# Optimization experiments

Hardware: AMD Instinct MI355X
Metric: run time of the kernel (lower is better)

Reference implementation:

```python
import jax, jax.numpy as jnp
import numpy as np

EMB = 1024
HEADS = 16
HEAD_DIM = EMB // HEADS
EPS = 1e-5


def setup_inputs() -> dict:
    key = jax.random.key(0)
    ks = jax.random.split(key, 10)
    B, T, D = 2, 2048, EMB
    s = 1.0 / np.sqrt(D)
    inp = {
        "x": jax.random.normal(ks[0], (B, T, D), dtype=jnp.float32),
        "wq": jax.random.normal(ks[1], (D, D), dtype=jnp.float32) * s,
        "bq": jnp.zeros((D,), jnp.float32),
        "wk": jax.random.normal(ks[2], (D, D), dtype=jnp.float32) * s,
        "bk": jnp.zeros((D,), jnp.float32),
        "wv": jax.random.normal(ks[3], (D, D), dtype=jnp.float32) * s,
        "bv": jnp.zeros((D,), jnp.float32),
        "wo": jax.random.normal(ks[4], (D, D), dtype=jnp.float32) * s,
        "bo": jnp.zeros((D,), jnp.float32),
        "gamma": jnp.ones((D,), jnp.float32),
        "beta": jnp.zeros((D,), jnp.float32),
    }
    return inp


def _attention(x, wq, bq, wk, bk, wv, bv, wo, bo, gamma, beta):
    B, T, D = x.shape
    H, Hd = HEADS, HEAD_DIM
    q = (x @ wq + bq).reshape(B, T, H, Hd)
    k = (x @ wk + bk).reshape(B, T, H, Hd)
    v = (x @ wv + bv).reshape(B, T, H, Hd)
    # scores: [B, H, T, T]
    scores = jnp.einsum("bthd,bshd->bhts", q, k) / np.sqrt(Hd)
    attn = jax.nn.softmax(scores, axis=-1)  # dropout is identity in eval
    ctx = jnp.einsum("bhts,bshd->bthd", attn, v).reshape(B, T, D)
    out = ctx @ wo + bo
    y = x + out  # residual (dropout identity)
    mu = jnp.mean(y, axis=-1, keepdims=True)
    var = jnp.var(y, axis=-1, keepdims=True)
    return (y - mu) * jax.lax.rsqrt(var + EPS) * gamma + beta


def reference(x, wq, bq, wk, bk, wv, bv, wo, bo, gamma, beta):
    return _attention(x, wq, bq, wk, bk, wv, bv, wo, bo, gamma, beta)
```

## Files before the change

### kernel.cpp

```cpp
#include <hip/hip_runtime.h>

#define BSZ   2
#define TSEQ  2048
#define DMOD  1024
#define NHEAD 16
#define HDIM  64
#define MROW  (BSZ*TSEQ)
#define LNEPS 1e-5f
#define QSCALE 0.18033688011f

typedef __bf16 bf16x8 __attribute__((ext_vector_type(8)));
typedef float  f32x4  __attribute__((ext_vector_type(4)));
typedef unsigned short us8 __attribute__((ext_vector_type(8)));
typedef unsigned short us4 __attribute__((ext_vector_type(4)));

__device__ __forceinline__ unsigned short f2bf(float f) {
    unsigned u = __float_as_uint(f);
    u += 0x7FFF + ((u >> 16) & 1);
    return (unsigned short)(u >> 16);
}
__device__ __forceinline__ float bf2f(unsigned short u) {
    return __uint_as_float((unsigned)u << 16);
}

__device__ __forceinline__ float fexp2(float x) {
#if __has_builtin(__builtin_amdgcn_exp2f)
    return __builtin_amdgcn_exp2f(x);
#else
    return __expf(x * 0.6931471805599453f);
#endif
}

__device__ __forceinline__ void gld_lds16(const void* g, void* l) {
    __builtin_amdgcn_global_load_lds(
        (const __attribute__((address_space(1))) unsigned int*)g,
        (__attribute__((address_space(3))) unsigned int*)l, 16, 0, 0);
}

__global__ __launch_bounds__(256) void prep_k(
    const float* __restrict__ x,
    const float* __restrict__ wq, const float* __restrict__ wk,
    const float* __restrict__ wv, const float* __restrict__ wo,
    unsigned short* __restrict__ Xb,
    unsigned short* __restrict__ WqkvT, unsigned short* __restrict__ WoT)
{
    const int tid = threadIdx.x;
    if (blockIdx.x < 2048) {
        const size_t i = ((size_t)blockIdx.x * 256 + tid) * 8;
        float4 a = *(const float4*)&x[i];
        float4 b = *(const float4*)&x[i + 4];
        union { unsigned short u[8]; uint4 v; } o;
        o.u[0]=f2bf(a.x); o.u[1]=f2bf(a.y); o.u[2]=f2bf(a.z); o.u[3]=f2bf(a.w);
        o.u[4]=f2bf(b.x); o.u[5]=f2bf(b.y); o.u[6]=f2bf(b.z); o.u[7]=f2bf(b.w);
        *(uint4*)&Xb[i] = o.v;
        return;
    }
    __shared__ float T[64][68];
    const int id = blockIdx.x - 2048;
    const int z  = id >> 8;
    const int bx = id & 15;
    const int by = (id >> 4) & 15;
    const float* W = (z == 0) ? wq : (z == 1) ? wk : (z == 2) ? wv : wo;
    unsigned short* Wt = (z < 3) ? (WqkvT + (size_t)z*1024*1024) : WoT;
    const int lr = tid >> 4, lc = (tid & 15) * 4;
    #pragma unroll
    for (int p = 0; p < 4; ++p) {
        const int kk = p*16 + lr;
        float4 v = *(const float4*)&W[(size_t)(by*64 + kk)*1024 + bx*64 + lc];
        T[lc+0][kk] = v.x; T[lc+1][kk] = v.y; T[lc+2][kk] = v.z; T[lc+3][kk] = v.w;
    }
    __syncthreads();
    #pragma unroll
    for (int p = 0; p < 2; ++p) {
        const int nl = p*32 + (tid >> 3);
        const int kb = (tid & 7) * 8;
        float4 a = *(const float4*)&T[nl][kb];
        float4 b = *(const float4*)&T[nl][kb+4];
        union { unsigned short u[8]; uint4 v; } o;
        o.u[0]=f2bf(a.x); o.u[1]=f2bf(a.y); o.u[2]=f2bf(a.z); o.u[3]=f2bf(a.w);
        o.u[4]=f2bf(b.x); o.u[5]=f2bf(b.y); o.u[6]=f2bf(b.z); o.u[7]=f2bf(b.w);
        *(uint4*)&Wt[(size_t)(bx*64 + nl)*1024 + by*64 + kb] = o.v;
    }
}

struct GemmFrags {
    const unsigned short* Ag[4]; const unsigned short* Bg[4];
    unsigned short *la[4], *lb[4];
    const unsigned short *ap[4][2], *bp[4][2];
};

__device__ __forceinline__ void gemm_setup(
    GemmFrags& F, unsigned short* As, unsigned short* Bs,
    const unsigned short* A, const unsigned short* Bt,
    int bm, int bn, int lda)
{
    const int tid  = threadIdx.x;
    const int wv   = tid >> 6;
    const int lane = tid & 63;
    const int quad = lane >> 4;
    const int l16  = lane & 15;
    const int wm   = wv & 1, wn = wv >> 1;
    const int r_l = lane >> 3;
    const int c_l = lane & 7;
    #pragma unroll
    for (int s = 0; s < 4; ++s) {
        const int i = wv*4 + s;
        const int R = i*8 + r_l;
        const int gc = (c_l ^ (R & 7)) * 8;
        F.Ag[s] = A  + (size_t)(bm + R)*lda + gc;
        F.Bg[s] = Bt + (size_t)(bn + R)*lda + gc;
        F.la[s] = As + i*512;
        F.lb[s] = Bs + i*512;
    }
    #pragma unroll
    for (int t = 0; t < 4; ++t)
        #pragma unroll
        for (int kh = 0; kh < 2; ++kh) {
            const int ra = wm*64 + t*16 + l16;
            const int rb = wn*64 + t*16 + l16;
            F.ap[t][kh] = &As[ra*64 + ((kh*4 + quad) ^ (ra & 7))*8];
            F.bp[t][kh] = &Bs[rb*64 + ((kh*4 + quad) ^ (rb & 7))*8];
        }
}

template<int SWAP>
__device__ __forceinline__ void gemm_kloop(
    GemmFrags& F, f32x4 (&acc)[4][4], int k_begin, int k_end)
{
    for (int k0 = k_begin; k0 < k_end; k0 += 64) {
        __syncthreads();
        #pragma unroll
        for (int s = 0; s < 4; ++s) {
            gld_lds16(F.Ag[s] + k0, F.la[s]);
            gld_lds16(F.Bg[s] + k0, F.lb[s]);
        }
        __syncthreads();
        #pragma unroll
        for (int kh = 0; kh < 2; ++kh) {
            bf16x8 af[4], bfr[4];
            #pragma unroll
            for (int t = 0; t < 4; ++t) {
                af[t]  = *(const bf16x8*)F.ap[t][kh];
                bfr[t] = *(const bf16x8*)F.bp[t][kh];
            }
            #pragma unroll
            for (int i = 0; i < 4; ++i)
                #pragma unroll
                for (int j = 0; j < 4; ++j)
                    acc[i][j] = SWAP
                        ? __builtin_amdgcn_mfma_f32_16x16x32_bf16(bfr[j], af[i], acc[i][j], 0, 0, 0)
                        : __builtin_amdgcn_mfma_f32_16x16x32_bf16(af[i], bfr[j], acc[i][j], 0, 0, 0);
        }
    }
}

__global__ __launch_bounds__(256) void gemm_qkv_k(
    const unsigned short* __restrict__ A, const unsigned short* __restrict__ Bt,
    const float* __restrict__ b0, const float* __restrict__ b1,
    const float* __restrict__ b2,
    unsigned short* __restrict__ oQ, unsigned short* __restrict__ oK,
    unsigned short* __restrict__ oV)
{
    __shared__ unsigned short As[128*64];
    __shared__ unsigned short Bs[128*64];
    const int tid  = threadIdx.x;
    const int wv   = tid >> 6;
    const int lane = tid & 63;
    const int quad = lane >> 4;
    const int l16  = lane & 15;
    const int wm   = wv & 1, wn = wv >> 1;
    const int bm = blockIdx.y * 128, bn = blockIdx.x * 128;

    GemmFrags F;
    gemm_setup(F, As, Bs, A, Bt, bm, bn, 1024);

    f32x4 acc[4][4];
    #pragma unroll
    for (int i = 0; i < 4; ++i)
        #pragma unroll
        for (int j = 0; j < 4; ++j) acc[i][j] = (f32x4){0.f,0.f,0.f,0.f};

    const int seg = bn >> 10;
    const float* bias = (seg == 0) ? b0 : (seg == 1) ? b1 : b2;
    const int cb = bn & 1023;

    if (seg < 2) {
        gemm_kloop<1>(F, acc, 0, 1024);
        unsigned short* O = (seg == 0) ? oQ : oK;
        const float sc = (seg == 0) ? QSCALE : 1.0f;
        #pragma unroll
        for (int mt = 0; mt < 4; ++mt) {
            const int m = bm + wm*64 + mt*16 + l16;
            #pragma unroll
            for (int nt = 0; nt < 4; ++nt) {
                const int n0 = cb + wn*64 + nt*16 + quad*4;
                const f32x4 bs = *(const f32x4*)&bias[n0];
                us4 o;
                #pragma unroll
                for (int r = 0; r < 4; ++r) o[r] = f2bf((acc[mt][nt][r] + bs[r]) * sc);
                *(us4*)&O[(size_t)m*1024 + n0] = o;
            }
        }
    } else {
        gemm_kloop<0>(F, acc, 0, 1024);
        #pragma unroll
        for (int nt = 0; nt < 4; ++nt) {
            const int ch = cb + wn*64 + nt*16 + l16;
            const float bs = bias[ch];
            #pragma unroll
            for (int mt = 0; mt < 4; ++mt) {
                const int grow0 = bm + wm*64 + mt*16 + quad*4;
                us4 o;
                #pragma unroll
                for (int r = 0; r < 4; ++r) o[r] = f2bf(acc[mt][nt][r] + bs);
                *(us4*)&oV[(size_t)ch*MROW + grow0] = o;
            }
        }
    }
}

__global__ __launch_bounds__(256) void gemm_proj_k(
    const unsigned short* __restrict__ A, const unsigned short* __restrict__ Bt,
    unsigned short* __restrict__ P)
{
    __shared__ unsigned short As[128*64];
    __shared__ unsigned short Bs[128*64];
    const int tid  = threadIdx.x;
    const int wv   = tid >> 6;
    const int lane = tid & 63;
    const int quad = lane >> 4;
    const int l16  = lane & 15;
    const int wm   = wv & 1, wn = wv >> 1;
    const int bm = blockIdx.y * 128, bn = blockIdx.x * 128;
    const int kz = blockIdx.z;

    GemmFrags F;
    gemm_setup(F, As, Bs, A, Bt, bm, bn, 1024);

    f32x4 acc[4][4];
    #pragma unroll
    for (int i = 0; i < 4; ++i)
        #pragma unroll
        for (int j = 0; j < 4; ++j) acc[i][j] = (f32x4){0.f,0.f,0.f,0.f};

    gemm_kloop<1>(F, acc, kz*512, kz*512 + 512);

    unsigned short* O = P + (size_t)kz*MROW*1024;
    #pragma unroll
    for (int mt = 0; mt < 4; ++mt) {
        const int m = bm + wm*64 + mt*16 + l16;
        #pragma unroll
        for (int nt = 0; nt < 4; ++nt) {
            const int n0 = bn + wn*64 + nt*16 + quad*4;
            us4 o;
            #pragma unroll
            for (int r = 0; r < 4; ++r) o[r] = f2bf(acc[mt][nt][r]);
            *(us4*)&O[(size_t)m*1024 + n0] = o;
        }
    }
}

__global__ __launch_bounds__(256, 2) void attn_k(
    const unsigned short* __restrict__ Qg,
    const unsigned short* __restrict__ Kg,
    const unsigned short* __restrict__ Vtg,
    unsigned short* __restrict__ CTX)
{
    __shared__ __align__(16) char lds_raw[51200];
    unsigned short* Qs = (unsigned short*)lds_raw;
    unsigned short* Ks = (unsigned short*)(lds_raw + 18432);
    unsigned short* Vs = (unsigned short*)(lds_raw + 34816);
    float* Od = (float*)lds_raw;
    float* Ld = (float*)(lds_raw + 34816);

    const int tid  = threadIdx.x;
    const int wv   = tid >> 6;
    const int lane = tid & 63;
    const int quad = lane >> 4;
    const int l16  = lane & 15;
    const int wq   = wv & 1;
    const int wk   = wv >> 1;
    const int qb   = blockIdx.x * 128;
    const int h    = blockIdx.y;
    const int b    = blockIdx.z;

    {
        const int row = tid & 127, cb = (tid >> 7) * 32;
        const unsigned short* Qrow = Qg + ((size_t)(b*TSEQ + qb + row))*DMOD + h*HDIM + cb;
        #pragma unroll
        for (int j = 0; j < 4; ++j)
            *(us8*)&Qs[row*72 + cb + j*8] = *(const us8*)&Qrow[j*8];
    }
    __syncthreads();
    bf16x8 qf[4][2];
    #pragma unroll
    for (int nt = 0; nt < 4; ++nt)
        #pragma unroll
        for (int kh = 0; kh < 2; ++kh)
            qf[nt][kh] = *(const bf16x8*)&Qs[(wq*64 + nt*16 + l16)*72 + kh*32 + quad*8];

    const int sr = lane >> 3;
    const int sc = lane & 7;
    const bool isK = (wv < 2);
    const int half = wv & 1;
    const unsigned short* gbase;
    unsigned int goff[8];
    unsigned short* ldst;
    if (isK) {
        gbase = Kg + ((size_t)(b*TSEQ + half*1024))*DMOD + h*HDIM;
        #pragma unroll
        for (int s = 0; s < 8; ++s) {
            const int R = s*8 + sr;
            const int gc = sc ^ ((R ^ (R >> 2)) & 7);
            goff[s] = (unsigned)(R*DMOD + gc*8);
        }
        ldst = Ks + half*4096;
    } else {
        gbase = Vtg + ((size_t)(h*HDIM))*MROW + b*TSEQ + half*1024;
        #pragma unroll
        for (int s = 0; s < 8; ++s) {
            const int D = s*8 + sr;
            const int gc = sc ^ (D & 7);
            goff[s] = (unsigned)(D*MROW + gc*8);
        }
        ldst = Vs + half*4096;
    }
    const size_t gstep = isK ? (size_t)64*DMOD : (size_t)64;

    const int rowA_l = (l16 >> 2)*8 + (l16 & 3);
    const int rowB_l = rowA_l + 4;
    const int swA = (rowA_l ^ (rowA_l >> 2)) & 7;
    const int swB = (rowB_l ^ (rowB_l >> 2)) & 7;
    const unsigned short* KsW = Ks + wk*4096;
    const unsigned short* VsW = Vs + wk*4096;

    bf16x8 onef;
    { union { unsigned short u[8]; bf16x8 v; } o1;
      #pragma unroll
      for (int i = 0; i < 8; ++i) o1.u[i] = 0x3F80;
      onef = o1.v; }

    f32x4 oacc[4][4];
    f32x4 lacc[4];
    #pragma unroll
    for (int dt = 0; dt < 4; ++dt)
        #pragma unroll
        for (int nt = 0; nt < 4; ++nt) oacc[dt][nt] = (f32x4){0.f,0.f,0.f,0.f};
    #pragma unroll
    for (int nt = 0; nt < 4; ++nt) lacc[nt] = (f32x4){0.f,0.f,0.f,0.f};

    for (int it = 0; it < 16; ++it) {
        __syncthreads();
        #pragma unroll
        for (int s = 0; s < 8; ++s)
            gld_lds16(gbase + (size_t)it*gstep + goff[s], ldst + s*512);
        __syncthreads();

        #pragma unroll
        for (int gl = 0; gl < 2; ++gl) {
            const int rA = gl*32 + rowA_l;
            const int rB = gl*32 + rowB_l;
            bf16x8 ka0 = *(const bf16x8*)&KsW[rA*64 + ((quad     ^ swA))*8];
            bf16x8 ka1 = *(const bf16x8*)&KsW[rA*64 + (((4+quad) ^ swA))*8];
            bf16x8 kb0 = *(const bf16x8*)&KsW[rB*64 + ((quad     ^ swB))*8];
            bf16x8 kb1 = *(const bf16x8*)&KsW[rB*64 + (((4+quad) ^ swB))*8];
            bf16x8 vf[4];
            #pragma unroll
            for (int dt = 0; dt < 4; ++dt)
                vf[dt] = *(const bf16x8*)&VsW[(dt*16 + l16)*64 + ((gl*4 + quad) ^ (l16 & 7))*8];

            #pragma unroll
            for (int nt = 0; nt < 4; ++nt) {
                f32x4 z = (f32x4){0.f,0.f,0.f,0.f};
                z = __builtin_amdgcn_mfma_f32_16x16x32_bf16(ka0, qf[nt][0], z, 0, 0, 0);
                f32x4 sA = __builtin_amdgcn_mfma_f32_16x16x32_bf16(ka1, qf[nt][1], z, 0, 0, 0);
                z = (f32x4){0.f,0.f,0.f,0.f};
                z = __builtin_amdgcn_mfma_f32_16x16x32_bf16(kb0, qf[nt][0], z, 0, 0, 0);
                f32x4 sB = __builtin_amdgcn_mfma_f32_16x16x32_bf16(kb1, qf[nt][1], z, 0, 0, 0);

                float eA[4], eB[4];
                #pragma unroll
                for (int r = 0; r < 4; ++r) { eA[r] = fexp2(sA[r]); eB[r] = fexp2(sB[r]); }
                union { unsigned d[4]; bf16x8 v; } up;
                up.d[0] = __builtin_amdgcn_perm(__float_as_uint(eA[1]), __float_as_uint(eA[0]), 0x07060302);
                up.d[1] = __builtin_amdgcn_perm(__float_as_uint(eA[3]), __float_as_uint(eA[2]), 0x07060302);
                up.d[2] = __builtin_amdgcn_perm(__float_as_uint(eB[1]), __float_as_uint(eB[0]), 0x07060302);
                up.d[3] = __builtin_amdgcn_perm(__float_as_uint(eB[3]), __float_as_uint(eB[2]), 0x07060302);
                const bf16x8 pf = up.v;

                lacc[nt] = __builtin_amdgcn_mfma_f32_16x16x32_bf16(onef, pf, lacc[nt], 0, 0, 0);
                #pragma unroll
                for (int dt = 0; dt < 4; ++dt)
                    oacc[dt][nt] = __builtin_amdgcn_mfma_f32_16x16x32_bf16(vf[dt], pf, oacc[dt][nt], 0, 0, 0);
            }
        }
    }

    __syncthreads();
    if (wk == 0) {
        float* od = Od + wq*64*68;
        #pragma unroll
        for (int nt = 0; nt < 4; ++nt) {
            #pragma unroll
            for (int dt = 0; dt < 4; ++dt)
                *(f32x4*)&od[(nt*16 + l16)*68 + dt*16 + quad*4] = oacc[dt][nt];
            if (quad == 0) Ld[wq*64 + nt*16 + l16] = lacc[nt][0];
        }
    }
    __syncthreads();
    if (wk == 1) {
        const float* od = Od + wq*64*68;
        #pragma unroll
        for (int nt = 0; nt < 4; ++nt) {
            const float l = Ld[wq*64 + nt*16 + l16] + lacc[nt][0];
            const float inv = 1.f / l;
            const int q = qb + wq*64 + nt*16 + l16;
            unsigned short* crow = CTX + ((size_t)(b*TSEQ + q))*DMOD + h*HDIM;
            #pragma unroll
            for (int dt = 0; dt < 4; ++dt) {
                f32x4 p = *(const f32x4*)&od[(nt*16 + l16)*68 + dt*16 + quad*4];
                us4 o;
                #pragma unroll
                for (int r = 0; r < 4; ++r) o[r] = f2bf((p[r] + oacc[dt][nt][r]) * inv);
                *(us4*)&crow[dt*16 + quad*4] = o;
            }
        }
    }
}

__global__ __launch_bounds__(256) void red_ln_k(
    const float* __restrict__ x, const unsigned short* __restrict__ P,
    const float* __restrict__ bo,
    const float* __restrict__ gamma, const float* __restrict__ beta,
    float* __restrict__ out)
{
    __shared__ float rs[4], rss[4];
    const int row = blockIdx.x;
    const int tid = threadIdx.x;
    const int c = tid * 4;
    const float4 xv = *(const float4*)&x[(size_t)row*DMOD + c];
    const us4 p0 = *(const us4*)&P[(size_t)row*DMOD + c];
    const us4 p1 = *(const us4*)&P[(size_t)(MROW + row)*DMOD + c];
    const float4 bv4 = *(const float4*)&bo[c];
    const float v0 = xv.x + bf2f(p0[0]) + bf2f(p1[0]) + bv4.x;
    const float v1 = xv.y + bf2f(p0[1]) + bf2f(p1[1]) + bv4.y;
    const float v2 = xv.z + bf2f(p0[2]) + bf2f(p1[2]) + bv4.z;
    const float v3 = xv.w + bf2f(p0[3]) + bf2f(p1[3]) + bv4.w;
    float s  = v0 + v1 + v2 + v3;
    float ss = v0*v0 + v1*v1 + v2*v2 + v3*v3;
    #pragma unroll
    for (int o = 32; o > 0; o >>= 1) {
        s  += __shfl_down(s,  o, 64);
        ss += __shfl_down(ss, o, 64);
    }
    if ((tid & 63) == 0) { rs[tid >> 6] = s; rss[tid >> 6] = ss; }
    __syncthreads();
    s  = rs[0] + rs[1] + rs[2] + rs[3];
    ss = rss[0] + rss[1] + rss[2] + rss[3];
    const float mean = s * (1.f/DMOD);
    const float var  = ss * (1.f/DMOD) - mean*mean;
    const float rstd = rsqrtf(var + LNEPS);
    const float4 gv = *(const float4*)&gamma[c];
    const float4 bv = *(const float4*)&beta[c];
    float4 o;
    o.x = (v0 - mean)*rstd*gv.x + bv.x;
    o.y = (v1 - mean)*rstd*gv.y + bv.y;
    o.z = (v2 - mean)*rstd*gv.z + bv.z;
    o.w = (v3 - mean)*rstd*gv.w + bv.w;
    *(float4*)&out[(size_t)row*DMOD + c] = o;
}

extern "C" void kernel_launch(void* const* d_in, const int* in_sizes, int n_in,
                              void* d_out, int out_size, void* d_ws, size_t ws_size,
                              hipStream_t stream) {
    const float* x     = (const float*)d_in[0];
    const float* wq    = (const float*)d_in[1];
    const float* bq    = (const float*)d_in[2];
    const float* wk    = (const float*)d_in[3];
    const float* bk    = (const float*)d_in[4];
    const float* wvp   = (const float*)d_in[5];
    const float* bvp   = (const float*)d_in[6];
    const float* wo    = (const float*)d_in[7];
    const float* bo    = (const float*)d_in[8];
    const float* gamma = (const float*)d_in[9];
    const float* beta  = (const float*)d_in[10];
    float* out = (float*)d_out;

    unsigned short* Xb    = (unsigned short*)d_ws;
    unsigned short* WqkvT = Xb    + (size_t)MROW*DMOD;
    unsigned short* WoT   = WqkvT + (size_t)3072*1024;
    unsigned short* Qb    = WoT   + (size_t)1024*1024;
    unsigned short* Kb    = Qb    + (size_t)MROW*DMOD;
    unsigned short* VtG   = Kb    + (size_t)MROW*DMOD;
    unsigned short* CTXb  = VtG   + (size_t)DMOD*MROW;
    unsigned short* Pp    = Qb;

    prep_k<<<3072, 256, 0, stream>>>(x, wq, wk, wvp, wo, Xb, WqkvT, WoT);

    gemm_qkv_k<<<dim3(3072/128, MROW/128), 256, 0, stream>>>(
        Xb, WqkvT, bq, bk, bvp, Qb, Kb, VtG);

    attn_k<<<dim3(TSEQ/128, NHEAD, BSZ), 256, 0, stream>>>(Qb, Kb, VtG, CTXb);

    gemm_proj_k<<<dim3(DMOD/128, MROW/128, 2), 256, 0, stream>>>(CTXb, WoT, Pp);

    red_ln_k<<<MROW, 256, 0, stream>>>(x, Pp, bo, gamma, beta, out);
}
```

Before: 201.0 us.

## Double-buffer GEMM k-loop with 32-wide LDS stages to overlap loads and MFMA

Splits each 64-wide K step of the QKV and projection GEMMs into two 32-wide stages held in two LDS buffers. The global-to-LDS load of the next stage is issued before the MFMA work on the current stage, so memory latency can overlap with compute instead of being serialized behind a barrier. The LDS swizzle and fragment offsets are reworked for the 32-column stage layout, and total LDS use stays the same. The loop still has two barriers per 64 of K, and the narrower stages mean fewer MFMAs between syncs.

New measurement: 206.1 us. +2.6%, slower.

```diff
diff --git a/kernel.cpp b/kernel.cpp
--- a/kernel.cpp
+++ b/kernel.cpp
@@ -84,14 +84,13 @@
 }
 
 struct GemmFrags {
-    const unsigned short* Ag[4]; const unsigned short* Bg[4];
-    unsigned short *la[4], *lb[4];
-    const unsigned short *ap[4][2], *bp[4][2];
+    const unsigned short* Ag[2]; const unsigned short* Bg[2];
+    int ldso[2];
+    int apo[4], bpo[4];
 };
 
 __device__ __forceinline__ void gemm_setup(
-    GemmFrags& F, unsigned short* As, unsigned short* Bs,
-    const unsigned short* A, const unsigned short* Bt,
+    GemmFrags& F, const unsigned short* A, const unsigned short* Bt,
     int bm, int bn, int lda)
 {
     const int tid  = threadIdx.x;
@@ -100,57 +99,69 @@
     const int quad = lane >> 4;
     const int l16  = lane & 15;
     const int wm   = wv & 1, wn = wv >> 1;
-    const int r_l = lane >> 3;
-    const int c_l = lane & 7;
-    #pragma unroll
-    for (int s = 0; s < 4; ++s) {
-        const int i = wv*4 + s;
-        const int R = i*8 + r_l;
-        const int gc = (c_l ^ (R & 7)) * 8;
+    const int r_l = lane >> 2;
+    const int c_l = lane & 3;
+    #pragma unroll
+    for (int s = 0; s < 2; ++s) {
+        const int R = wv*32 + s*16 + r_l;
+        const int gc = (c_l ^ (r_l & 3)) * 8;
         F.Ag[s] = A  + (size_t)(bm + R)*lda + gc;
         F.Bg[s] = Bt + (size_t)(bn + R)*lda + gc;
-        F.la[s] = As + i*512;
-        F.lb[s] = Bs + i*512;
-    }
-    #pragma unroll
-    for (int t = 0; t < 4; ++t)
-        #pragma unroll
-        for (int kh = 0; kh < 2; ++kh) {
-            const int ra = wm*64 + t*16 + l16;
-            const int rb = wn*64 + t*16 + l16;
-            F.ap[t][kh] = &As[ra*64 + ((kh*4 + quad) ^ (ra & 7))*8];
-            F.bp[t][kh] = &Bs[rb*64 + ((kh*4 + quad) ^ (rb & 7))*8];
-        }
+        F.ldso[s] = (wv*32 + s*16)*32;
+    }
+    #pragma unroll
+    for (int t = 0; t < 4; ++t) {
+        const int ra = wm*64 + t*16 + l16;
+        const int rb = wn*64 + t*16 + l16;
+        F.apo[t] = ra*32 + ((quad ^ (ra & 3))*8);
+        F.bpo[t] = rb*32 + ((quad ^ (rb & 3))*8);
+    }
+}
+
+__device__ __forceinline__ void gemm_load(
+    GemmFrags& F, unsigned short* SA, unsigned short* SB, int k0)
+{
+    #pragma unroll
+    for (int s = 0; s < 2; ++s) {
+        gld_lds16(F.Ag[s] + k0, SA + F.ldso[s]);
+        gld_lds16(F.Bg[s] + k0, SB + F.ldso[s]);
+    }
+}
+
+template<int SWAP>
+__device__ __forceinline__ void gemm_compute(
+    GemmFrags& F, const unsigned short* SA, const unsigned short* SB,
+    f32x4 (&acc)[4][4])
+{
+    bf16x8 af[4], bfr[4];
+    #pragma unroll
+    for (int t = 0; t < 4; ++t) {
+        af[t]  = *(const bf16x8*)(SA + F.apo[t]);
+        bfr[t] = *(const bf16x8*)(SB + F.bpo[t]);
+    }
+    #pragma unroll
+    for (int i = 0; i < 4; ++i)
+        #pragma unroll
+        for (int j = 0; j < 4; ++j)
+            acc[i][j] = SWAP
+                ? __builtin_amdgcn_mfma_f32_16x16x32_bf16(bfr[j], af[i], acc[i][j], 0, 0, 0)
+                : __builtin_amdgcn_mfma_f32_16x16x32_bf16(af[i], bfr[j], acc[i][j], 0, 0, 0);
 }
 
 template<int SWAP>
 __device__ __forceinline__ void gemm_kloop(
-    GemmFrags& F, f32x4 (&acc)[4][4], int k_begin, int k_end)
-{
-    for (int k0 = k_begin; k0 < k_end; k0 += 64) {
+    GemmFrags& F, unsigned short* S, f32x4 (&acc)[4][4], int kb, int ke)
+{
+    unsigned short* A0 = S;         unsigned short* A1 = S + 4096;
+    unsigned short* B0 = S + 8192;  unsigned short* B1 = S + 12288;
+    gemm_load(F, A0, B0, kb);
+    for (int k0 = kb; k0 < ke; k0 += 64) {
         __syncthreads();
-        #pragma unroll
-        for (int s = 0; s < 4; ++s) {
-            gld_lds16(F.Ag[s] + k0, F.la[s]);
-            gld_lds16(F.Bg[s] + k0, F.lb[s]);
-        }
+        gemm_load(F, A1, B1, k0 + 32);
+        gemm_compute<SWAP>(F, A0, B0, acc);
         __syncthreads();
-        #pragma unroll
-        for (int kh = 0; kh < 2; ++kh) {
-            bf16x8 af[4], bfr[4];
-            #pragma unroll
-            for (int t = 0; t < 4; ++t) {
-                af[t]  = *(const bf16x8*)F.ap[t][kh];
-                bfr[t] = *(const bf16x8*)F.bp[t][kh];
-            }
-            #pragma unroll
-            for (int i = 0; i < 4; ++i)
-                #pragma unroll
-                for (int j = 0; j < 4; ++j)
-                    acc[i][j] = SWAP
-                        ? __builtin_amdgcn_mfma_f32_16x16x32_bf16(bfr[j], af[i], acc[i][j], 0, 0, 0)
-                        : __builtin_amdgcn_mfma_f32_16x16x32_bf16(af[i], bfr[j], acc[i][j], 0, 0, 0);
-        }
+        if (k0 + 64 < ke) gemm_load(F, A0, B0, k0 + 64);
+        gemm_compute<SWAP>(F, A1, B1, acc);
     }
 }
 
@@ -161,8 +172,7 @@
     unsigned short* __restrict__ oQ, unsigned short* __restrict__ oK,
     unsigned short* __restrict__ oV)
 {
-    __shared__ unsigned short As[128*64];
-    __shared__ unsigned short Bs[128*64];
+    __shared__ unsigned short S[4*4096];
     const int tid  = threadIdx.x;
     const int wv   = tid >> 6;
     const int lane = tid & 63;
@@ -172,7 +182,7 @@
     const int bm = blockIdx.y * 128, bn = blockIdx.x * 128;
 
     GemmFrags F;
-    gemm_setup(F, As, Bs, A, Bt, bm, bn, 1024);
+    gemm_setup(F, A, Bt, bm, bn, 1024);
 
     f32x4 acc[4][4];
     #pragma unroll
@@ -185,7 +195,7 @@
     const int cb = bn & 1023;
 
     if (seg < 2) {
-        gemm_kloop<1>(F, acc, 0, 1024);
+        gemm_kloop<1>(F, S, acc, 0, 1024);
         unsigned short* O = (seg == 0) ? oQ : oK;
         const float sc = (seg == 0) ? QSCALE : 1.0f;
         #pragma unroll
@@ -202,7 +212,7 @@
             }
         }
     } else {
-        gemm_kloop<0>(F, acc, 0, 1024);
+        gemm_kloop<0>(F, S, acc, 0, 1024);
         #pragma unroll
         for (int nt = 0; nt < 4; ++nt) {
             const int ch = cb + wn*64 + nt*16 + l16;
@@ -223,8 +233,7 @@
     const unsigned short* __restrict__ A, const unsigned short* __restrict__ Bt,
     unsigned short* __restrict__ P)
 {
-    __shared__ unsigned short As[128*64];
-    __shared__ unsigned short Bs[128*64];
+    __shared__ unsigned short S[4*4096];
     const int tid  = threadIdx.x;
     const int wv   = tid >> 6;
     const int lane = tid & 63;
@@ -235,7 +244,7 @@
     const int kz = blockIdx.z;
 
     GemmFrags F;
-    gemm_setup(F, As, Bs, A, Bt, bm, bn, 1024);
+    gemm_setup(F, A, Bt, bm, bn, 1024);
 
     f32x4 acc[4][4];
     #pragma unroll
@@ -243,7 +252,7 @@
         #pragma unroll
         for (int j = 0; j < 4; ++j) acc[i][j] = (f32x4){0.f,0.f,0.f,0.f};
 
-    gemm_kloop<1>(F, acc, kz*512, kz*512 + 512);
+    gemm_kloop<1>(F, S, acc, kz*512, kz*512 + 512);
 
     unsigned short* O = P + (size_t)kz*MROW*1024;
     #pragma unroll
```
